# Kernel tuning notes

Hardware: AMD Instinct MI355X
Metric: run time of the kernel (lower is better)

The kernel has to match this reference:

```python
import jax, jax.numpy as jnp
import numpy as np

EMB = 128  # emb_dim (D)
HID = 2 * EMB  # MLPKernel hidden width (2D, since kernel input is concat[Phi_A, Phi_B])


def setup_inputs() -> dict:
    key = jax.random.key(0)
    ks = jax.random.split(key, 8)
    B, N, D = 2, 512, EMB
    s1 = 1.0 / np.sqrt(2 * D)
    s2 = 1.0 / np.sqrt(HID)
    return {
        "Phi_A": jax.random.normal(ks[0], (B, N, D), jnp.float32),
        "Phi_B": jax.random.normal(ks[1], (B, N, D), jnp.float32),
        # MLPKernel params: Linear(2D->2D) -> ReLU -> Linear(2D->2D) -> ReLU -> Linear(2D->1)
        "W1": jax.random.normal(ks[2], (2 * D, HID), jnp.float32) * s1,
        "b1": jnp.zeros((HID,), jnp.float32),
        "W2": jax.random.normal(ks[3], (HID, HID), jnp.float32) * s2,
        "b2": jnp.zeros((HID,), jnp.float32),
        "W3": jax.random.normal(ks[4], (HID, 1), jnp.float32) * s2,
        "b3": jnp.zeros((1,), jnp.float32),
    }


def reference(Phi_A, Phi_B, W1, b1, W2, b2, W3, b3):
    # Faithful to: kernel(cat[Phi_A_r, Phi_B_r]) over all N*N pairs -> dro [B,N,N].
    # First linear on concat == split-weight matmuls + broadcast add (same math,
    # avoids materializing the [B,N,N,2D] repeated tensor).
    D = Phi_A.shape[-1]
    hA = jnp.einsum("bnd,dh->bnh", Phi_A, W1[:D])   # [B,N,H]
    hB = jnp.einsum("bmd,dh->bmh", Phi_B, W1[D:])   # [B,M,H]
    h = jax.nn.relu(hA[:, :, None, :] + hB[:, None, :, :] + b1)  # [B,N,M,H]
    h = jax.nn.relu(jnp.einsum("bnmh,hk->bnmk", h, W2) + b2)      # [B,N,M,H]
    dro = (jnp.einsum("bnmh,hk->bnmk", h, W3) + b3)[..., 0]       # [B,N,M]
    return dro
```

## Files before the change

kernel.cpp:

```cpp
#include <hip/hip_runtime.h>
#include <hip/hip_bf16.h>

#define BB 2
#define NN 512
#define DD 128
#define HH 256

typedef __attribute__((ext_vector_type(4))) float    f32x4;
typedef __attribute__((ext_vector_type(8))) _Float16 f16x8;
typedef __attribute__((ext_vector_type(4))) int      i32x4;

union F16x8 {
  f16x8 v;
  i32x4 i;
};

template <int CTRL>
__device__ __forceinline__ float dpp_add(float x) {
  int s = __builtin_amdgcn_update_dpp(0, __float_as_int(x), CTRL, 0xF, 0xF, true);
  return x + __int_as_float(s);
}

#define S1_ROWS 8
#define S1_BLOCKS (2 * (BB * NN) / S1_ROWS)
__global__ __launch_bounds__(256) void stage1(
    const float* __restrict__ PhiA, const float* __restrict__ PhiB,
    const float* __restrict__ W1,  const float* __restrict__ b1,
    const float* __restrict__ W2,
    _Float16* __restrict__ hA, _Float16* __restrict__ hB,
    _Float16* __restrict__ W2t) {
  if (blockIdx.x >= S1_BLOCKS) {
    const int bid2 = blockIdx.x - S1_BLOCKS;
    const int col  = bid2 * 32 + (threadIdx.x >> 3);
    const int k0   = (threadIdx.x & 7) * 32;
#pragma unroll
    for (int j = 0; j < 32; j++)
      W2t[col * HH + k0 + j] = (_Float16)W2[(k0 + j) * HH + col];
    return;
  }
  __shared__ float phis[S1_ROWS * DD];
  const int side = blockIdx.x & 1;
  const int row0 = (blockIdx.x >> 1) * S1_ROWS;
  const float* Phi = side ? PhiB : PhiA;
  const float* W   = W1 + side * DD * HH;
  ((f32x4*)phis)[threadIdx.x] =
      ((const f32x4*)(Phi + (size_t)row0 * DD))[threadIdx.x];
  __syncthreads();
  const int h = threadIdx.x;
  float acc[S1_ROWS];
#pragma unroll
  for (int i = 0; i < S1_ROWS; i++) acc[i] = 0.f;
  for (int d0 = 0; d0 < DD; d0 += 4) {
    const float w0 = W[(d0 + 0) * HH + h];
    const float w1 = W[(d0 + 1) * HH + h];
    const float w2 = W[(d0 + 2) * HH + h];
    const float w3 = W[(d0 + 3) * HH + h];
#pragma unroll
    for (int i = 0; i < S1_ROWS; i++) {
      f32x4 ph = *(const f32x4*)&phis[i * DD + d0];
      acc[i] = fmaf(ph.x, w0, acc[i]);
      acc[i] = fmaf(ph.y, w1, acc[i]);
      acc[i] = fmaf(ph.z, w2, acc[i]);
      acc[i] = fmaf(ph.w, w3, acc[i]);
    }
  }
  const float bias = side ? 0.f : b1[h];
  _Float16* o = (side ? hB : hA) + (size_t)row0 * HH + h;
#pragma unroll
  for (int i = 0; i < S1_ROWS; i++) o[i * HH] = (_Float16)(acc[i] + bias);
}

#define GRID_MAIN 512
#define KITERS 32

__global__ __launch_bounds__(512, 4) void pairmlp(
    const _Float16* __restrict__ hA, const _Float16* __restrict__ hB,
    const _Float16* __restrict__ W2t, const float* __restrict__ b2,
    const float* __restrict__ W3, const float* __restrict__ b3,
    float* __restrict__ out) {
  __shared__ __align__(16) short h1[2][32 * 256];
  __shared__ float red[2][8][32];

  const int tid  = threadIdx.x;
  const int lane = tid & 63;
  const int w    = tid >> 6;
  const int g    = lane >> 4;
  const int lr   = lane & 15;
  const int bid  = blockIdx.x;
  const int bb    = bid >> 8;
  const int m0    = ((bid >> 3) & 31) * 16;
  const int nbase = bid & 7;

  f16x8 breg[8][2];
#pragma unroll
  for (int ks = 0; ks < 8; ks++)
#pragma unroll
    for (int ct = 0; ct < 2; ct++) {
      const int col = w * 32 + ct * 16 + lr;
      breg[ks][ct] = *reinterpret_cast<const f16x8*>(&W2t[col * HH + ks * 32 + g * 8]);
    }
  float b2v[2], w3v[2];
#pragma unroll
  for (int ct = 0; ct < 2; ct++) {
    const int col = w * 32 + ct * 16 + lr;
    b2v[ct] = b2[col];
    w3v[ct] = W3[col];
  }
  const float b3v = b3[0];

  const int p  = tid >> 4;
  const int c4 = tid & 15;

  F16x8 hbr[2];
  {
    const _Float16* hBp = hB + ((size_t)(bb * NN + m0 + (p & 15))) * HH + c4 * 16;
#pragma unroll
    for (int q = 0; q < 2; q++)
      hbr[q].v = *reinterpret_cast<const f16x8*>(hBp + q * 8);
  }
  const _Float16* hAbase = hA + ((size_t)(bb * NN + (p >> 4))) * HH + c4 * 16;

  auto loadA = [&](int n0, F16x8* av) {
    const _Float16* hAp = hAbase + (size_t)n0 * HH;
#pragma unroll
    for (int q = 0; q < 2; q++)
      av[q].v = *reinterpret_cast<const f16x8*>(hAp + q * 8);
  };
  auto build = [&](const F16x8* av, int buf) {
    const f16x8 zero8 = {};
#pragma unroll
    for (int q = 0; q < 2; q++) {
      F16x8 r;
      r.v = __builtin_elementwise_max(av[q].v + hbr[q].v, zero8);
      const int addr = (p * 512 + c4 * 32 + q * 16) ^ ((p & 7) << 4);
      *reinterpret_cast<i32x4*>(reinterpret_cast<char*>(h1[buf]) + addr) = r.i;
    }
  };

  {
    F16x8 av[2];
    loadA(2 * nbase, av);
    build(av, 0);
  }

  for (int k = 0; k < KITERS; k++) {
    const int cur = k & 1;
    const int n0  = 2 * (nbase + 8 * k);
    __syncthreads();

    F16x8 av[2];
    if (k < KITERS - 1) loadA(n0 + 16, av);

    if (k > 0 && tid < 32) {
      const int pb = cur ^ 1;
      float v = b3v;
#pragma unroll
      for (int ww = 0; ww < 8; ww++) v += red[pb][ww][tid];
      const int n = (n0 - 16) + (tid >> 4);
      out[((size_t)(bb * NN + n)) * NN + m0 + (tid & 15)] = v;
    }

    f32x4 acc[2][2];
#pragma unroll
    for (int rt = 0; rt < 2; rt++)
#pragma unroll
      for (int ct = 0; ct < 2; ct++) acc[rt][ct] = (f32x4){0.f, 0.f, 0.f, 0.f};
#pragma unroll
    for (int ks = 0; ks < 8; ks++) {
      f16x8 afrag[2];
#pragma unroll
      for (int rt = 0; rt < 2; rt++) {
        const int row  = rt * 16 + lr;
        const int addr = (row * 512 + ks * 64 + g * 16) ^ ((row & 7) << 4);
        afrag[rt] = *reinterpret_cast<const f16x8*>(
            reinterpret_cast<const char*>(h1[cur]) + addr);
      }
#pragma unroll
      for (int rt = 0; rt < 2; rt++)
#pragma unroll
        for (int ct = 0; ct < 2; ct++)
          acc[rt][ct] = __builtin_amdgcn_mfma_f32_16x16x32_f16(
              afrag[rt], breg[ks][ct], acc[rt][ct], 0, 0, 0);
    }

    if (k < KITERS - 1) build(av, cur ^ 1);

    float part[2][4];
#pragma unroll
    for (int rt = 0; rt < 2; rt++)
#pragma unroll
      for (int r = 0; r < 4; r++) {
        float s = fmaxf(acc[rt][0][r] + b2v[0], 0.f) * w3v[0];
        s = fmaf(fmaxf(acc[rt][1][r] + b2v[1], 0.f), w3v[1], s);
        s = dpp_add<0xB1>(s);
        s = dpp_add<0x4E>(s);
        s = dpp_add<0x141>(s);
        s = dpp_add<0x140>(s);
        part[rt][r] = s;
      }
    if (lr == 0) {
#pragma unroll
      for (int rt = 0; rt < 2; rt++)
#pragma unroll
        for (int r = 0; r < 4; r++)
          red[cur][w][rt * 16 + g * 4 + r] = part[rt][r];
    }
  }

  __syncthreads();
  if (tid < 32) {
    const int pb = (KITERS - 1) & 1;
    float v = b3v;
#pragma unroll
    for (int ww = 0; ww < 8; ww++) v += red[pb][ww][tid];
    const int n = 2 * (nbase + 8 * (KITERS - 1)) + (tid >> 4);
    out[((size_t)(bb * NN + n)) * NN + m0 + (tid & 15)] = v;
  }
}

extern "C" void kernel_launch(void* const* d_in, const int* in_sizes, int n_in,
                              void* d_out, int out_size, void* d_ws, size_t ws_size,
                              hipStream_t stream) {
  const float* PhiA = (const float*)d_in[0];
  const float* PhiB = (const float*)d_in[1];
  const float* W1   = (const float*)d_in[2];
  const float* b1   = (const float*)d_in[3];
  const float* W2   = (const float*)d_in[4];
  const float* b2   = (const float*)d_in[5];
  const float* W3   = (const float*)d_in[6];
  const float* b3   = (const float*)d_in[7];
  float* out = (float*)d_out;

  char* ws = (char*)d_ws;
  _Float16* hA  = (_Float16*)ws;
  _Float16* hB  = (_Float16*)(ws + (512u << 10));
  _Float16* W2t = (_Float16*)(ws + (1024u << 10));

  hipLaunchKernelGGL(stage1, dim3(S1_BLOCKS + 8), dim3(256), 0, stream,
                     PhiA, PhiB, W1, b1, W2, hA, hB, W2t);
  hipLaunchKernelGGL(pairmlp, dim3(GRID_MAIN), dim3(512), 0, stream,
                     hA, hB, W2t, b2, W3, b3, out);
}
```

Measured before the change: 151.0 us.

## Build relu(hA+hB) fragments directly in registers, dropping the LDS staging buffer

The pair-sum activation is now computed per MFMA fragment in registers. hB is held in registers per lane and hA is read from global memory each k-step, so the shared-memory h1 double buffer and its swizzled writes and reads are gone. Each iteration handles one n-row (16 pairs) instead of two, with twice the loop iterations and a single barrier per iteration. This removes LDS traffic and the staging stores, at the cost of more global loads of hA on the critical path, half the MFMA work per barrier, and less independent MFMA work to hide latency.

```diff
diff --git a/kernel.cpp b/kernel.cpp
--- a/kernel.cpp
+++ b/kernel.cpp
@@ -9,11 +9,6 @@
 typedef __attribute__((ext_vector_type(4))) float    f32x4;
 typedef __attribute__((ext_vector_type(8))) _Float16 f16x8;
 typedef __attribute__((ext_vector_type(4))) int      i32x4;
-
-union F16x8 {
-  f16x8 v;
-  i32x4 i;
-};
 
 template <int CTRL>
 __device__ __forceinline__ float dpp_add(float x) {
@@ -71,15 +66,14 @@
 }
 
 #define GRID_MAIN 512
-#define KITERS 32
+#define KITERS 64
 
 __global__ __launch_bounds__(512, 4) void pairmlp(
     const _Float16* __restrict__ hA, const _Float16* __restrict__ hB,
     const _Float16* __restrict__ W2t, const float* __restrict__ b2,
     const float* __restrict__ W3, const float* __restrict__ b3,
     float* __restrict__ out) {
-  __shared__ __align__(16) short h1[2][32 * 256];
-  __shared__ float red[2][8][32];
+  __shared__ float red[2][8][16];
 
   const int tid  = threadIdx.x;
   const int lane = tid & 63;
@@ -97,8 +91,16 @@
 #pragma unroll
     for (int ct = 0; ct < 2; ct++) {
       const int col = w * 32 + ct * 16 + lr;
-      breg[ks][ct] = *reinterpret_cast<const f16x8*>(&W2t[col * HH + ks * 32 + g * 8]);
+      breg[ks][ct] =
+          *reinterpret_cast<const f16x8*>(&W2t[col * HH + ks * 32 + g * 8]);
     }
+  f16x8 hbr[8];
+  {
+    const _Float16* hBp = hB + (size_t)(bb * NN + m0 + lr) * HH + g * 8;
+#pragma unroll
+    for (int ks = 0; ks < 8; ks++)
+      hbr[ks] = *reinterpret_cast<const f16x8*>(hBp + ks * 32);
+  }
   float b2v[2], w3v[2];
 #pragma unroll
   for (int ct = 0; ct < 2; ct++) {
@@ -108,113 +110,53 @@
   }
   const float b3v = b3[0];
 
-  const int p  = tid >> 4;
-  const int c4 = tid & 15;
-
-  F16x8 hbr[2];
-  {
-    const _Float16* hBp = hB + ((size_t)(bb * NN + m0 + (p & 15))) * HH + c4 * 16;
-#pragma unroll
-    for (int q = 0; q < 2; q++)
-      hbr[q].v = *reinterpret_cast<const f16x8*>(hBp + q * 8);
-  }
-  const _Float16* hAbase = hA + ((size_t)(bb * NN + (p >> 4))) * HH + c4 * 16;
-
-  auto loadA = [&](int n0, F16x8* av) {
-    const _Float16* hAp = hAbase + (size_t)n0 * HH;
-#pragma unroll
-    for (int q = 0; q < 2; q++)
-      av[q].v = *reinterpret_cast<const f16x8*>(hAp + q * 8);
-  };
-  auto build = [&](const F16x8* av, int buf) {
-    const f16x8 zero8 = {};
-#pragma unroll
-    for (int q = 0; q < 2; q++) {
-      F16x8 r;
-      r.v = __builtin_elementwise_max(av[q].v + hbr[q].v, zero8);
-      const int addr = (p * 512 + c4 * 32 + q * 16) ^ ((p & 7) << 4);
-      *reinterpret_cast<i32x4*>(reinterpret_cast<char*>(h1[buf]) + addr) = r.i;
-    }
-  };
-
-  {
-    F16x8 av[2];
-    loadA(2 * nbase, av);
-    build(av, 0);
-  }
+  const _Float16* hAp = hA + (size_t)(bb * NN + nbase) * HH + g * 8;
+  const f16x8 zero8 = {};
 
   for (int k = 0; k < KITERS; k++) {
     const int cur = k & 1;
-    const int n0  = 2 * (nbase + 8 * k);
-    __syncthreads();
 
-    F16x8 av[2];
-    if (k < KITERS - 1) loadA(n0 + 16, av);
-
-    if (k > 0 && tid < 32) {
+    if (k > 0 && tid < 16) {
       const int pb = cur ^ 1;
       float v = b3v;
 #pragma unroll
       for (int ww = 0; ww < 8; ww++) v += red[pb][ww][tid];
-      const int n = (n0 - 16) + (tid >> 4);
-      out[((size_t)(bb * NN + n)) * NN + m0 + (tid & 15)] = v;
+      const int npr = nbase + 8 * (k - 1);
+      out[(size_t)(bb * NN + npr) * NN + m0 + tid] = v;
     }
 
-    f32x4 acc[2][2];
-#pragma unroll
-    for (int rt = 0; rt < 2; rt++)
-#pragma unroll
-      for (int ct = 0; ct < 2; ct++) acc[rt][ct] = (f32x4){0.f, 0.f, 0.f, 0.f};
+    const _Float16* hAk = hAp + (size_t)(8 * k) * HH;
+    f32x4 acc[2];
+    acc[0] = (f32x4){0.f, 0.f, 0.f, 0.f};
+    acc[1] = (f32x4){0.f, 0.f, 0.f, 0.f};
 #pragma unroll
     for (int ks = 0; ks < 8; ks++) {
-      f16x8 afrag[2];
-#pragma unroll
-      for (int rt = 0; rt < 2; rt++) {
-        const int row  = rt * 16 + lr;
-        const int addr = (row * 512 + ks * 64 + g * 16) ^ ((row & 7) << 4);
-        afrag[rt] = *reinterpret_cast<const f16x8*>(
-            reinterpret_cast<const char*>(h1[cur]) + addr);
-      }
-#pragma unroll
-      for (int rt = 0; rt < 2; rt++)
-#pragma unroll
-        for (int ct = 0; ct < 2; ct++)
-          acc[rt][ct] = __builtin_amdgcn_mfma_f32_16x16x32_f16(
-              afrag[rt], breg[ks][ct], acc[rt][ct], 0, 0, 0);
+      f16x8 ha = *reinterpret_cast<const f16x8*>(hAk + ks * 32);
+      f16x8 af = __builtin_elementwise_max(ha + hbr[ks], zero8);
+      acc[0] = __builtin_amdgcn_mfma_f32_16x16x32_f16(af, breg[ks][0], acc[0], 0, 0, 0);
+      acc[1] = __builtin_amdgcn_mfma_f32_16x16x32_f16(af, breg[ks][1], acc[1], 0, 0, 0);
     }
 
-    if (k < KITERS - 1) build(av, cur ^ 1);
-
-    float part[2][4];
 #pragma unroll
-    for (int rt = 0; rt < 2; rt++)
-#pragma unroll
-      for (int r = 0; r < 4; r++) {
-        float s = fmaxf(acc[rt][0][r] + b2v[0], 0.f) * w3v[0];
-        s = fmaf(fmaxf(acc[rt][1][r] + b2v[1], 0.f), w3v[1], s);
-        s = dpp_add<0xB1>(s);
-        s = dpp_add<0x4E>(s);
-        s = dpp_add<0x141>(s);
-        s = dpp_add<0x140>(s);
-        part[rt][r] = s;
-      }
-    if (lr == 0) {
-#pragma unroll
-      for (int rt = 0; rt < 2; rt++)
-#pragma unroll
-        for (int r = 0; r < 4; r++)
-          red[cur][w][rt * 16 + g * 4 + r] = part[rt][r];
+    for (int r = 0; r < 4; r++) {
+      float s = fmaxf(acc[0][r] + b2v[0], 0.f) * w3v[0];
+      s = fmaf(fmaxf(acc[1][r] + b2v[1], 0.f), w3v[1], s);
+      s = dpp_add<0xB1>(s);
+      s = dpp_add<0x4E>(s);
+      s = dpp_add<0x141>(s);
+      s = dpp_add<0x140>(s);
+      if (lr == 0) red[cur][w][g * 4 + r] = s;
     }
+    __syncthreads();
   }
 
-  __syncthreads();
-  if (tid < 32) {
+  if (tid < 16) {
     const int pb = (KITERS - 1) & 1;
     float v = b3v;
 #pragma unroll
     for (int ww = 0; ww < 8; ww++) v += red[pb][ww][tid];
-    const int n = 2 * (nbase + 8 * (KITERS - 1)) + (tid >> 4);
-    out[((size_t)(bb * NN + n)) * NN + m0 + (tid & 15)] = v;
+    const int nlast = nbase + 8 * (KITERS - 1);
+    out[(size_t)(bb * NN + nlast) * NN + m0 + tid] = v;
   }
 }
 
```

New measurement: 206.4 us. 36.7% more time.

## Transpose MFMA operands to simplify epilogue reduction; shrink stage1 rows per block

Applied to the files above, without the earlier changes.

Swaps the MFMA A/B operands so each lane holds outputs for one pair row across several hidden columns. The epilogue can then do bias+ReLU+W3 dot per lane, using max(acc,-b2)*w3 plus a precomputed constant in place of add-then-max. This replaces four DPP adds per element with two cross-lane shuffles per row tile and a simpler shared-memory write. Stage1 also drops to 2 rows per block with wider unrolling, giving more blocks but less weight reuse per block.

```diff
diff --git a/kernel.cpp b/kernel.cpp
--- a/kernel.cpp
+++ b/kernel.cpp
@@ -10,18 +10,9 @@
 typedef __attribute__((ext_vector_type(8))) _Float16 f16x8;
 typedef __attribute__((ext_vector_type(4))) int      i32x4;
 
-union F16x8 {
-  f16x8 v;
-  i32x4 i;
-};
-
-template <int CTRL>
-__device__ __forceinline__ float dpp_add(float x) {
-  int s = __builtin_amdgcn_update_dpp(0, __float_as_int(x), CTRL, 0xF, 0xF, true);
-  return x + __int_as_float(s);
-}
-
-#define S1_ROWS 8
+union F16x8 { f16x8 v; i32x4 i; };
+
+#define S1_ROWS 2
 #define S1_BLOCKS (2 * (BB * NN) / S1_ROWS)
 __global__ __launch_bounds__(256) void stage1(
     const float* __restrict__ PhiA, const float* __restrict__ PhiB,
@@ -43,31 +34,34 @@
   const int row0 = (blockIdx.x >> 1) * S1_ROWS;
   const float* Phi = side ? PhiB : PhiA;
   const float* W   = W1 + side * DD * HH;
-  ((f32x4*)phis)[threadIdx.x] =
-      ((const f32x4*)(Phi + (size_t)row0 * DD))[threadIdx.x];
+  if (threadIdx.x < (S1_ROWS * DD) / 4)
+    ((f32x4*)phis)[threadIdx.x] =
+        ((const f32x4*)(Phi + (size_t)row0 * DD))[threadIdx.x];
   __syncthreads();
   const int h = threadIdx.x;
-  float acc[S1_ROWS];
-#pragma unroll
-  for (int i = 0; i < S1_ROWS; i++) acc[i] = 0.f;
-  for (int d0 = 0; d0 < DD; d0 += 4) {
-    const float w0 = W[(d0 + 0) * HH + h];
-    const float w1 = W[(d0 + 1) * HH + h];
-    const float w2 = W[(d0 + 2) * HH + h];
-    const float w3 = W[(d0 + 3) * HH + h];
-#pragma unroll
-    for (int i = 0; i < S1_ROWS; i++) {
-      f32x4 ph = *(const f32x4*)&phis[i * DD + d0];
-      acc[i] = fmaf(ph.x, w0, acc[i]);
-      acc[i] = fmaf(ph.y, w1, acc[i]);
-      acc[i] = fmaf(ph.z, w2, acc[i]);
-      acc[i] = fmaf(ph.w, w3, acc[i]);
-    }
+  float acc0 = 0.f, acc1 = 0.f;
+#pragma unroll
+  for (int d0 = 0; d0 < DD; d0 += 8) {
+    float wv[8];
+#pragma unroll
+    for (int j = 0; j < 8; j++) wv[j] = W[(d0 + j) * HH + h];
+    f32x4 p0a = *(const f32x4*)&phis[d0];
+    f32x4 p0b = *(const f32x4*)&phis[d0 + 4];
+    f32x4 p1a = *(const f32x4*)&phis[DD + d0];
+    f32x4 p1b = *(const f32x4*)&phis[DD + d0 + 4];
+    acc0 = fmaf(p0a.x, wv[0], acc0); acc0 = fmaf(p0a.y, wv[1], acc0);
+    acc0 = fmaf(p0a.z, wv[2], acc0); acc0 = fmaf(p0a.w, wv[3], acc0);
+    acc0 = fmaf(p0b.x, wv[4], acc0); acc0 = fmaf(p0b.y, wv[5], acc0);
+    acc0 = fmaf(p0b.z, wv[6], acc0); acc0 = fmaf(p0b.w, wv[7], acc0);
+    acc1 = fmaf(p1a.x, wv[0], acc1); acc1 = fmaf(p1a.y, wv[1], acc1);
+    acc1 = fmaf(p1a.z, wv[2], acc1); acc1 = fmaf(p1a.w, wv[3], acc1);
+    acc1 = fmaf(p1b.x, wv[4], acc1); acc1 = fmaf(p1b.y, wv[5], acc1);
+    acc1 = fmaf(p1b.z, wv[6], acc1); acc1 = fmaf(p1b.w, wv[7], acc1);
   }
   const float bias = side ? 0.f : b1[h];
   _Float16* o = (side ? hB : hA) + (size_t)row0 * HH + h;
-#pragma unroll
-  for (int i = 0; i < S1_ROWS; i++) o[i * HH] = (_Float16)(acc[i] + bias);
+  o[0]  = (_Float16)(acc0 + bias);
+  o[HH] = (_Float16)(acc1 + bias);
 }
 
 #define GRID_MAIN 512
@@ -97,15 +91,21 @@
 #pragma unroll
     for (int ct = 0; ct < 2; ct++) {
       const int col = w * 32 + ct * 16 + lr;
-      breg[ks][ct] = *reinterpret_cast<const f16x8*>(&W2t[col * HH + ks * 32 + g * 8]);
-    }
-  float b2v[2], w3v[2];
-#pragma unroll
-  for (int ct = 0; ct < 2; ct++) {
-    const int col = w * 32 + ct * 16 + lr;
-    b2v[ct] = b2[col];
-    w3v[ct] = W3[col];
-  }
+      breg[ks][ct] =
+          *reinterpret_cast<const f16x8*>(&W2t[col * HH + ks * 32 + g * 8]);
+    }
+  float nb2[2][4], w3v[2][4];
+  float Kc = 0.f;
+#pragma unroll
+  for (int ct = 0; ct < 2; ct++)
+#pragma unroll
+    for (int r = 0; r < 4; r++) {
+      const int col = w * 32 + ct * 16 + g * 4 + r;
+      const float bv = b2[col], wv = W3[col];
+      nb2[ct][r] = -bv;
+      w3v[ct][r] = wv;
+      Kc = fmaf(bv, wv, Kc);
+    }
   const float b3v = b3[0];
 
   const int p  = tid >> 4;
@@ -180,30 +180,27 @@
 #pragma unroll
         for (int ct = 0; ct < 2; ct++)
           acc[rt][ct] = __builtin_amdgcn_mfma_f32_16x16x32_f16(
-              afrag[rt], breg[ks][ct], acc[rt][ct], 0, 0, 0);
+              breg[ks][ct], afrag[rt], acc[rt][ct], 0, 0, 0);
     }
 
     if (k < KITERS - 1) build(av, cur ^ 1);
 
-    float part[2][4];
-#pragma unroll
-    for (int rt = 0; rt < 2; rt++)
-#pragma unroll
-      for (int r = 0; r < 4; r++) {
-        float s = fmaxf(acc[rt][0][r] + b2v[0], 0.f) * w3v[0];
-        s = fmaf(fmaxf(acc[rt][1][r] + b2v[1], 0.f), w3v[1], s);
-        s = dpp_add<0xB1>(s);
-        s = dpp_add<0x4E>(s);
-        s = dpp_add<0x141>(s);
-        s = dpp_add<0x140>(s);
-        part[rt][r] = s;
-      }
-    if (lr == 0) {
-#pragma unroll
-      for (int rt = 0; rt < 2; rt++)
+    float s[2];
+#pragma unroll
+    for (int rt = 0; rt < 2; rt++) {
+      float t = Kc;
+#pragma unroll
+      for (int ct = 0; ct < 2; ct++)
 #pragma unroll
         for (int r = 0; r < 4; r++)
-          red[cur][w][rt * 16 + g * 4 + r] = part[rt][r];
+          t = fmaf(fmaxf(acc[rt][ct][r], nb2[ct][r]), w3v[ct][r], t);
+      t += __shfl_xor(t, 16);
+      t += __shfl_xor(t, 32);
+      s[rt] = t;
+    }
+    if (lane < 16) {
+      red[cur][w][lane]      = s[0];
+      red[cur][w][16 + lane] = s[1];
     }
   }
 
@@ -214,7 +211,7 @@
 #pragma unroll
     for (int ww = 0; ww < 8; ww++) v += red[pb][ww][tid];
     const int n = 2 * (nbase + 8 * (KITERS - 1)) + (tid >> 4);
-    out[((size_t)(bb * NN + n)) * NN + m0 + (tid & 15)] = v;
+    out[(size_t)(bb * NN + n) * NN + m0 + (tid & 15)] = v;
   }
 }
 
```

Result: slower. 223.1 us (+47.8%).
